# Kernel tuning notes

Hardware: AMD Instinct MI355X
Metric: run time of the kernel (lower is better)

Reference implementation:

```python
import jax, jax.numpy as jnp
import numpy as np

B, IN, H, OUT, RANK = 2048, 256, 128, 128, 8
EPS = 1e-5

def setup_inputs() -> dict:
    key = jax.random.key(0)
    ks = jax.random.split(key, 9)
    inv = lambda n: 1.0 / np.sqrt(n)
    return {
        "X": jax.random.normal(ks[0], (B, IN), jnp.float32),
        "W1": jax.random.uniform(ks[1], (IN, H), jnp.float32, -inv(IN), inv(IN)),
        "b1": jnp.zeros((H,), jnp.float32),
        "W2": jax.random.uniform(ks[2], (IN, OUT), jnp.float32, -inv(IN), inv(IN)),
        "b2": jnp.zeros((OUT,), jnp.float32),
        "W3": jax.random.uniform(ks[3], (H, OUT), jnp.float32, -inv(H), inv(H)),
        "b3": jnp.zeros((OUT,), jnp.float32),
        "P": jax.random.normal(ks[4], (RANK, H, H, H), jnp.float32),  # (rank, p, q, k)
        "gz": jnp.ones((H,), jnp.float32),
        "bz": jnp.zeros((H,), jnp.float32),
        "gy": jnp.ones((H,), jnp.float32),
        "by": jnp.zeros((H,), jnp.float32),
    }

def _bn(x, g, b):
    # training-mode BatchNorm1d: batch stats, biased variance
    m = x.mean(axis=0)
    v = x.var(axis=0)
    return (x - m) * jax.lax.rsqrt(v + EPS) * g + b

def reference(X, W1, b1, W2, b2, W3, b3, P, gz, bz, gy, by):
    Z = jax.nn.relu(X @ W1 + b1)               # (B, H); dropout = identity (eval)

    def step(carry, Pi):
        Zi, Y = carry
        # batch_quadratic: out[b,k] = sum_{p,q} Zi[b,p] * Pi[p,q,k] * Z[b,q]
        Zi = jnp.einsum('bp,pqk,bq->bk', Zi, Pi, Z)
        Zi = _bn(Zi, gz, bz)
        return (Zi, Y + Zi / RANK), None

    Y0 = jnp.zeros((X.shape[0], H), X.dtype)
    (_, Y), _ = jax.lax.scan(step, (Z, Y0), P)
    Y = _bn(Y, gy, by)
    out = jax.nn.relu(jax.nn.relu(Y @ W3 + b3) + jax.nn.relu(X @ W2 + b2))
    return out
```

## Files before the change

### kernel.cpp

```cpp
#include <hip/hip_runtime.h>

typedef __bf16 bf16x8 __attribute__((ext_vector_type(8)));
typedef float  floatx4 __attribute__((ext_vector_type(4)));

constexpr int B_    = 2048;
constexpr int NIN   = 256;
constexpr int H_    = 128;
constexpr int RANK_ = 8;
constexpr float EPS_ = 1e-5f;

__global__ __launch_bounds__(256)
void k_head(const float* __restrict__ X,
            const float* __restrict__ W1, const float* __restrict__ b1,
            const float* __restrict__ W2, const float* __restrict__ b2,
            const float* __restrict__ P,
            float* __restrict__ R2, __bf16* __restrict__ Zbf,
            __bf16* __restrict__ Pperm, float* __restrict__ stats ) {
    __shared__ float smem[4160];
    const int bx = blockIdx.x, t = threadIdx.x;

    if (bx < RANK_ + 1) stats[bx * 256 + t] = 0.f;

    if (bx < 512) {
        const int b0 = bx * 4;
#pragma unroll
        for (int i = 0; i < 4; ++i) {
            const int e = i * 256 + t;
            smem[e] = X[(size_t)(b0 + (e >> 8)) * NIN + (e & 255)];
        }
        __syncthreads();
        const int col = t & 127, rh = t >> 7;
        float s1a = 0.f, s2a = 0.f, s1b = 0.f, s2b = 0.f;
        const float* sxa = smem + rh * 256;
        const float* sxb = smem + (rh + 2) * 256;
#pragma unroll 8
        for (int i = 0; i < NIN; ++i) {
            const float w1 = W1[i * H_ + col];
            const float w2 = W2[i * H_ + col];
            s1a = fmaf(sxa[i], w1, s1a);  s2a = fmaf(sxa[i], w2, s2a);
            s1b = fmaf(sxb[i], w1, s1b);  s2b = fmaf(sxb[i], w2, s2b);
        }
        const int ba = b0 + rh, bb = b0 + rh + 2;
        const float za = fmaxf(s1a + b1[col], 0.f), ra = fmaxf(s2a + b2[col], 0.f);
        const float zb = fmaxf(s1b + b1[col], 0.f), rb = fmaxf(s2b + b2[col], 0.f);
        Zbf[(size_t)ba * H_ + col] = (__bf16)za;  R2[(size_t)ba * H_ + col] = ra;
        Zbf[(size_t)bb * H_ + col] = (__bf16)zb;  R2[(size_t)bb * H_ + col] = rb;
        __syncthreads();
    }
    {
        const int r = bx >> 7, p = bx & 127;
        const float4* Pp4 = (const float4*)(P + ((size_t)r * H_ + p) * (H_ * H_));
        __bf16* dst = Pperm + (size_t)r * (H_ * H_ * H_);
        const int L = t & 63, quad = L >> 4, lo = L & 15, g0 = t >> 6;
#pragma unroll
        for (int s = 0; s < 4; ++s) {
#pragma unroll
            for (int it = 0; it < 4; ++it) {
                const int idx = it * 256 + t;
                const int q = idx >> 5, k4 = idx & 31;
                const float4 v = Pp4[(size_t)(s * 32 + q) * 32 + k4];
                float* d = smem + q * 129 + k4 * 4;
                d[0] = v.x; d[1] = v.y; d[2] = v.z; d[3] = v.w;
            }
            __syncthreads();
#pragma unroll
            for (int gg = 0; gg < 2; ++gg) {
                const int g = g0 + 4 * gg;
                __bf16 v8[8];
#pragma unroll
                for (int j = 0; j < 8; ++j)
                    v8[j] = (__bf16)smem[(quad * 8 + j) * 129 + g * 16 + lo];
                *(bf16x8*)(dst + (((size_t)(g * 128 + p) * 4 + s) * 64 + L) * 8) =
                    *(const bf16x8*)v8;
            }
            __syncthreads();
        }
    }
}

__global__ __launch_bounds__(512, 2)
void k_rank(const __bf16* __restrict__ Pr, const __bf16* __restrict__ Zbf,
            const float* __restrict__ prevT, const float* __restrict__ prevStats,
            const float* __restrict__ gz, const float* __restrict__ bz,
            float* __restrict__ T, float* __restrict__ stats,
            float* __restrict__ Y, const int ymode) {
    __shared__ float smem[8960];
    const int kg = blockIdx.x, mblk = blockIdx.y, b0 = mblk * 64;
    const int t = threadIdx.x;
    const int w = t >> 6, L = t & 63, quad = L >> 4, lo = L & 15;

    float* sAl = smem + 8704; float* sBe = smem + 8832;
    if (ymode != 0 && t < 128) {
        const float s1 = prevStats[t], s2 = prevStats[128 + t];
        const float mm = s1 * (1.f / B_);
        const float var = s2 * (1.f / B_) - mm * mm;
        const float a = rsqrtf(var + EPS_) * gz[t];
        sAl[t] = a; sBe[t] = bz[t] - mm * a;
    }
    bf16x8 A[4][4];
#pragma unroll
    for (int mt = 0; mt < 4; ++mt)
#pragma unroll
        for (int ks = 0; ks < 4; ++ks)
            A[mt][ks] = *(const bf16x8*)(Zbf + (size_t)(b0 + mt * 16 + lo) * H_ + ks * 32 + quad * 8);

    const bf16x8* Pb = (const bf16x8*)Pr;
    const int p0 = w * 16;
    const size_t fbase = ((size_t)kg * 128 + p0) * 4;
    bf16x8 Bf[4], Bn[4];
#pragma unroll
    for (int s = 0; s < 4; ++s) Bf[s] = Pb[(fbase + s) * 64 + L];

    __syncthreads();
    {
        const int sp = t & 127, rr = t >> 7;
        if (ymode == 0) {
#pragma unroll
            for (int i = 0; i < 16; ++i) {
                const int row = rr + 4 * i;
                smem[sp * 68 + row] = (float)Zbf[(size_t)(b0 + row) * H_ + sp];
            }
        } else {
            const float a = sAl[sp], be = sBe[sp];
#pragma unroll
            for (int i = 0; i < 16; ++i) {
                const int row = rr + 4 * i;
                const float zin = fmaf(prevT[(size_t)(b0 + row) * H_ + sp], a, be);
                smem[sp * 68 + row] = zin;
                if (kg == 0) {
                    float* yp = Y + (size_t)(b0 + row) * H_ + sp;
                    *yp = (ymode == 1) ? zin * (1.f / RANK_) : fmaf(zin, 1.f / RANK_, *yp);
                }
            }
        }
    }
    __syncthreads();

    floatx4 acc[4];
#pragma unroll
    for (int mt = 0; mt < 4; ++mt) acc[mt] = (floatx4){0.f, 0.f, 0.f, 0.f};

    for (int pp = 0; pp < 16; ++pp) {
        const int p = p0 + pp;
        if (pp < 15) {
#pragma unroll
            for (int s = 0; s < 4; ++s)
                Bn[s] = Pb[(fbase + (size_t)(pp + 1) * 4 + s) * 64 + L];
        }
        floatx4 S[4];
#pragma unroll
        for (int mt = 0; mt < 4; ++mt) S[mt] = (floatx4){0.f, 0.f, 0.f, 0.f};
#pragma unroll
        for (int ks = 0; ks < 4; ++ks)
#pragma unroll
            for (int mt = 0; mt < 4; ++mt)
                S[mt] = __builtin_amdgcn_mfma_f32_16x16x32_bf16(A[mt][ks], Bf[ks], S[mt], 0, 0, 0);
#pragma unroll
        for (int mt = 0; mt < 4; ++mt) {
            const floatx4 zi = *(const floatx4*)&smem[p * 68 + mt * 16 + quad * 4];
            acc[mt] += zi * S[mt];
        }
#pragma unroll
        for (int s = 0; s < 4; ++s) Bf[s] = Bn[s];
    }
    __syncthreads();
#pragma unroll
    for (int mt = 0; mt < 4; ++mt)
#pragma unroll
        for (int i = 0; i < 4; ++i)
            smem[w * 1024 + (mt * 4 + i) * 64 + L] = acc[mt][i];
    if (t < 32) smem[8192 + t] = 0.f;
    __syncthreads();

    float cs = 0.f, cs2 = 0.f;
#pragma unroll
    for (int k2 = 0; k2 < 2; ++k2) {
        const int e = t + 512 * k2;
        float v = 0.f;
#pragma unroll
        for (int q = 0; q < 8; ++q) v += smem[q * 1024 + e];
        const int j = e >> 6, L2 = e & 63;
        const int row = b0 + (j >> 2) * 16 + (L2 >> 4) * 4 + (j & 3);
        const int col = kg * 16 + (L2 & 15);
        T[(size_t)row * H_ + col] = v;
        cs += v; cs2 += v * v;
    }
    cs  += __shfl_xor(cs, 16);  cs  += __shfl_xor(cs, 32);
    cs2 += __shfl_xor(cs2, 16); cs2 += __shfl_xor(cs2, 32);
    if (L < 16) { atomicAdd(&smem[8192 + L], cs); atomicAdd(&smem[8208 + L], cs2); }
    __syncthreads();
    if (t < 16)      atomicAdd(&stats[kg * 16 + t],            smem[8192 + t]);
    else if (t < 32) atomicAdd(&stats[128 + kg * 16 + t - 16], smem[8192 + t]);
}

__global__ __launch_bounds__(256)
void k_y(const float* __restrict__ T7, const float* __restrict__ s7,
         const float* __restrict__ gz, const float* __restrict__ bz,
         float* __restrict__ Y, float* __restrict__ ysums) {
    __shared__ float sAl[128], sBe[128], red[256];
    const int bx = blockIdx.x, t = threadIdx.x;
    if (t < 128) {
        const float s1 = s7[t], s2 = s7[128 + t];
        const float mm = s1 * (1.f / B_);
        const float var = s2 * (1.f / B_) - mm * mm;
        const float a = rsqrtf(var + EPS_) * gz[t];
        sAl[t] = a; sBe[t] = bz[t] - mm * a;
    }
    red[t] = 0.f;
    __syncthreads();
    const int col = t & 127, half = t >> 7;
    const float a = sAl[col], be = sBe[col];
    float ps = 0.f, ps2 = 0.f;
    for (int i = 0; i < 16; ++i) {
        const int b = bx * 32 + half + 2 * i;
        const size_t gi = (size_t)b * H_ + col;
        const float y = Y[gi] + fmaf(T7[gi], a, be) * (1.f / RANK_);
        Y[gi] = y;
        ps += y; ps2 += y * y;
    }
    atomicAdd(&red[col],       half == 0 ? ps  : 0.f);
    atomicAdd(&red[128 + col], half == 0 ? ps2 : 0.f);
    __syncthreads();
    atomicAdd(&red[col],       half == 1 ? ps  : 0.f);
    atomicAdd(&red[128 + col], half == 1 ? ps2 : 0.f);
    __syncthreads();
    if (t < 128) {
        atomicAdd(&ysums[t],       red[t]);
        atomicAdd(&ysums[128 + t], red[128 + t]);
    }
}

__global__ __launch_bounds__(256)
void k_out(const float* __restrict__ Y, const float* __restrict__ ystats,
           const float* __restrict__ gy, const float* __restrict__ by,
           const float* __restrict__ W3, const float* __restrict__ b3,
           const float* __restrict__ R2, float* __restrict__ out) {
    __shared__ float sy[8 * 132];
    const int bx = blockIdx.x, t = threadIdx.x;
    const int col = t & 127, rh = t >> 7;
    const int b0 = bx * 8;
    const float mm = ystats[col] * (1.f / B_);
    const float var = ystats[128 + col] * (1.f / B_) - mm * mm;
    const float ay = rsqrtf(var + EPS_) * gy[col];
    const float bb = by[col] - mm * ay;
#pragma unroll
    for (int i = 0; i < 4; ++i) {
        const int row = rh + 2 * i;
        sy[row * 132 + col] = fmaf(Y[(size_t)(b0 + row) * H_ + col], ay, bb);
    }
    __syncthreads();
#pragma unroll
    for (int j = 0; j < 4; ++j) {
        const int row = rh * 4 + j;
        float s = 0.f;
        const float* syr = sy + row * 132;
#pragma unroll 8
        for (int h = 0; h < H_; ++h)
            s = fmaf(syr[h], W3[h * H_ + col], s);
        const size_t gi = (size_t)(b0 + row) * H_ + col;
        out[gi] = fmaxf(fmaxf(s + b3[col], 0.f) + R2[gi], 0.f);
    }
}

extern "C" void kernel_launch(void* const* d_in, const int* in_sizes, int n_in,
                              void* d_out, int out_size, void* d_ws, size_t ws_size,
                              hipStream_t stream) {
    const float* X  = (const float*)d_in[0];
    const float* W1 = (const float*)d_in[1];
    const float* b1 = (const float*)d_in[2];
    const float* W2 = (const float*)d_in[3];
    const float* b2 = (const float*)d_in[4];
    const float* W3 = (const float*)d_in[5];
    const float* b3 = (const float*)d_in[6];
    const float* P  = (const float*)d_in[7];
    const float* gz = (const float*)d_in[8];
    const float* bz = (const float*)d_in[9];
    const float* gy = (const float*)d_in[10];
    const float* by = (const float*)d_in[11];
    float* out = (float*)d_out;

    const size_t rankElems = (size_t)H_ * H_ * H_;

    char* wsb = (char*)d_ws;
    float* R2     = (float*)wsb;   wsb += (size_t)B_ * H_ * 4;
    float* Y      = (float*)wsb;   wsb += (size_t)B_ * H_ * 4;
    float* stats  = (float*)wsb;   wsb += (size_t)(RANK_ + 1) * 256 * 4;
    float* T      = (float*)wsb;   wsb += (size_t)RANK_ * B_ * H_ * 4;
    __bf16* Zbf   = (__bf16*)wsb;  wsb += (size_t)B_ * H_ * 2;
    __bf16* Pperm = (__bf16*)wsb;

    float* ysums = stats + RANK_ * 256;

    k_head<<<1024, 256, 0, stream>>>(X, W1, b1, W2, b2, P, R2, Zbf, Pperm, stats);

    for (int r = 0; r < RANK_; ++r) {
        const float* prevT = (r == 0) ? (const float*)Zbf : (T + (size_t)(r - 1) * B_ * H_);
        const float* prevS = (r == 0) ? stats : (stats + (r - 1) * 256);
        const int ymode = (r == 0) ? 0 : (r == 1 ? 1 : 2);
        k_rank<<<dim3(8, 32), 512, 0, stream>>>(Pperm + (size_t)r * rankElems, Zbf,
                                                prevT, prevS, gz, bz,
                                                T + (size_t)r * B_ * H_, stats + r * 256,
                                                Y, ymode);
    }

    k_y<<<64, 256, 0, stream>>>(T + (size_t)7 * B_ * H_, stats + 7 * 256, gz, bz, Y, ysums);
    k_out<<<256, 256, 0, stream>>>(Y, ysums, gy, by, W3, b3, R2, out);
}
```

Before: 313.7 us.

## Move Y accumulation out of rank kernels into final k_y pass over all ranks

Removes the per-rank Y read-modify-write done by the kg==0 blocks in k_rank, which serialised extra global traffic onto one column of blocks. k_y now recomputes all eight BN-normalised rank outputs from the stored T buffers and their stats and sums them in one pass. In k_head the P-permute loads all 16 float4s into registers up front to overlap global loads and drops one barrier per stage. k_rank also moves its smem staging ahead of the first B-fragment loads. The cost is that k_y reads eight T planes instead of one, and k_head uses more registers.

```diff
diff --git a/kernel.cpp b/kernel.cpp
--- a/kernel.cpp
+++ b/kernel.cpp
@@ -52,15 +52,24 @@
         const float4* Pp4 = (const float4*)(P + ((size_t)r * H_ + p) * (H_ * H_));
         __bf16* dst = Pperm + (size_t)r * (H_ * H_ * H_);
         const int L = t & 63, quad = L >> 4, lo = L & 15, g0 = t >> 6;
-#pragma unroll
-        for (int s = 0; s < 4; ++s) {
+
+        float4 rg[4][4];
+#pragma unroll
+        for (int s = 0; s < 4; ++s)
 #pragma unroll
             for (int it = 0; it < 4; ++it) {
                 const int idx = it * 256 + t;
-                const int q = idx >> 5, k4 = idx & 31;
-                const float4 v = Pp4[(size_t)(s * 32 + q) * 32 + k4];
-                float* d = smem + q * 129 + k4 * 4;
-                d[0] = v.x; d[1] = v.y; d[2] = v.z; d[3] = v.w;
+                rg[s][it] = Pp4[(size_t)(s * 32 + (idx >> 5)) * 32 + (idx & 31)];
+            }
+#pragma unroll
+        for (int s = 0; s < 4; ++s) {
+            if (s) __syncthreads();
+#pragma unroll
+            for (int it = 0; it < 4; ++it) {
+                const int idx = it * 256 + t;
+                float* d = smem + (idx >> 5) * 129 + (idx & 31) * 4;
+                d[0] = rg[s][it].x; d[1] = rg[s][it].y;
+                d[2] = rg[s][it].z; d[3] = rg[s][it].w;
             }
             __syncthreads();
 #pragma unroll
@@ -73,7 +82,6 @@
                 *(bf16x8*)(dst + (((size_t)(g * 128 + p) * 4 + s) * 64 + L) * 8) =
                     *(const bf16x8*)v8;
             }
-            __syncthreads();
         }
     }
 }
@@ -82,15 +90,14 @@
 void k_rank(const __bf16* __restrict__ Pr, const __bf16* __restrict__ Zbf,
             const float* __restrict__ prevT, const float* __restrict__ prevStats,
             const float* __restrict__ gz, const float* __restrict__ bz,
-            float* __restrict__ T, float* __restrict__ stats,
-            float* __restrict__ Y, const int ymode) {
+            float* __restrict__ T, float* __restrict__ stats, const int first) {
     __shared__ float smem[8960];
     const int kg = blockIdx.x, mblk = blockIdx.y, b0 = mblk * 64;
     const int t = threadIdx.x;
     const int w = t >> 6, L = t & 63, quad = L >> 4, lo = L & 15;
 
     float* sAl = smem + 8704; float* sBe = smem + 8832;
-    if (ymode != 0 && t < 128) {
+    if (!first && t < 128) {
         const float s1 = prevStats[t], s2 = prevStats[128 + t];
         const float mm = s1 * (1.f / B_);
         const float var = s2 * (1.f / B_) - mm * mm;
@@ -103,6 +110,29 @@
 #pragma unroll
         for (int ks = 0; ks < 4; ++ks)
             A[mt][ks] = *(const bf16x8*)(Zbf + (size_t)(b0 + mt * 16 + lo) * H_ + ks * 32 + quad * 8);
+    __syncthreads();
+    {
+        const int sp = t & 127, rr = t >> 7;
+        if (first) {
+#pragma unroll
+            for (int i = 0; i < 16; ++i) {
+                const int row = rr + 4 * i;
+                smem[sp * 68 + row] = (float)Zbf[(size_t)(b0 + row) * H_ + sp];
+            }
+        } else {
+            const float a = sAl[sp], be = sBe[sp];
+#pragma unroll
+            for (int i = 0; i < 16; ++i) {
+                const int row = rr + 4 * i;
+                smem[sp * 68 + row] = fmaf(prevT[(size_t)(b0 + row) * H_ + sp], a, be);
+            }
+        }
+    }
+    __syncthreads();
+
+    floatx4 acc[4];
+#pragma unroll
+    for (int mt = 0; mt < 4; ++mt) acc[mt] = (floatx4){0.f, 0.f, 0.f, 0.f};
 
     const bf16x8* Pb = (const bf16x8*)Pr;
     const int p0 = w * 16;
@@ -110,35 +140,6 @@
     bf16x8 Bf[4], Bn[4];
 #pragma unroll
     for (int s = 0; s < 4; ++s) Bf[s] = Pb[(fbase + s) * 64 + L];
-
-    __syncthreads();
-    {
-        const int sp = t & 127, rr = t >> 7;
-        if (ymode == 0) {
-#pragma unroll
-            for (int i = 0; i < 16; ++i) {
-                const int row = rr + 4 * i;
-                smem[sp * 68 + row] = (float)Zbf[(size_t)(b0 + row) * H_ + sp];
-            }
-        } else {
-            const float a = sAl[sp], be = sBe[sp];
-#pragma unroll
-            for (int i = 0; i < 16; ++i) {
-                const int row = rr + 4 * i;
-                const float zin = fmaf(prevT[(size_t)(b0 + row) * H_ + sp], a, be);
-                smem[sp * 68 + row] = zin;
-                if (kg == 0) {
-                    float* yp = Y + (size_t)(b0 + row) * H_ + sp;
-                    *yp = (ymode == 1) ? zin * (1.f / RANK_) : fmaf(zin, 1.f / RANK_, *yp);
-                }
-            }
-        }
-    }
-    __syncthreads();
-
-    floatx4 acc[4];
-#pragma unroll
-    for (int mt = 0; mt < 4; ++mt) acc[mt] = (floatx4){0.f, 0.f, 0.f, 0.f};
 
     for (int pp = 0; pp < 16; ++pp) {
         const int p = p0 + pp;
@@ -194,28 +195,32 @@
 }
 
 __global__ __launch_bounds__(256)
-void k_y(const float* __restrict__ T7, const float* __restrict__ s7,
+void k_y(const float* __restrict__ T, const float* __restrict__ sums,
          const float* __restrict__ gz, const float* __restrict__ bz,
          float* __restrict__ Y, float* __restrict__ ysums) {
-    __shared__ float sAl[128], sBe[128], red[256];
+    __shared__ float al[1024], be[1024], red[256];
     const int bx = blockIdx.x, t = threadIdx.x;
-    if (t < 128) {
-        const float s1 = s7[t], s2 = s7[128 + t];
+    for (int e = t; e < 1024; e += 256) {
+        const int rr = e >> 7, k = e & 127;
+        const float s1 = sums[rr * 256 + k], s2 = sums[rr * 256 + 128 + k];
         const float mm = s1 * (1.f / B_);
         const float var = s2 * (1.f / B_) - mm * mm;
-        const float a = rsqrtf(var + EPS_) * gz[t];
-        sAl[t] = a; sBe[t] = bz[t] - mm * a;
+        const float a = rsqrtf(var + EPS_) * gz[k];
+        al[e] = a; be[e] = bz[k] - mm * a;
     }
     red[t] = 0.f;
     __syncthreads();
     const int col = t & 127, half = t >> 7;
-    const float a = sAl[col], be = sBe[col];
     float ps = 0.f, ps2 = 0.f;
     for (int i = 0; i < 16; ++i) {
         const int b = bx * 32 + half + 2 * i;
-        const size_t gi = (size_t)b * H_ + col;
-        const float y = Y[gi] + fmaf(T7[gi], a, be) * (1.f / RANK_);
-        Y[gi] = y;
+        float y = 0.f;
+#pragma unroll
+        for (int rr = 0; rr < 8; ++rr)
+            y += fmaf(T[(size_t)rr * B_ * H_ + (size_t)b * H_ + col],
+                      al[rr * 128 + col], be[rr * 128 + col]);
+        y *= (1.f / RANK_);
+        Y[(size_t)b * H_ + col] = y;
         ps += y; ps2 += y * y;
     }
     atomicAdd(&red[col],       half == 0 ? ps  : 0.f);
@@ -296,13 +301,12 @@
     for (int r = 0; r < RANK_; ++r) {
         const float* prevT = (r == 0) ? (const float*)Zbf : (T + (size_t)(r - 1) * B_ * H_);
         const float* prevS = (r == 0) ? stats : (stats + (r - 1) * 256);
-        const int ymode = (r == 0) ? 0 : (r == 1 ? 1 : 2);
         k_rank<<<dim3(8, 32), 512, 0, stream>>>(Pperm + (size_t)r * rankElems, Zbf,
                                                 prevT, prevS, gz, bz,
                                                 T + (size_t)r * B_ * H_, stats + r * 256,
-                                                Y, ymode);
-    }
-
-    k_y<<<64, 256, 0, stream>>>(T + (size_t)7 * B_ * H_, stats + 7 * 256, gz, bz, Y, ysums);
+                                                r == 0 ? 1 : 0);
+    }
+
+    k_y<<<64, 256, 0, stream>>>(T, stats, gz, bz, Y, ysums);
     k_out<<<256, 256, 0, stream>>>(Y, ysums, gy, by, W3, b3, R2, out);
 }
```

New measurement: 268.4 us. -14.4%, faster.
